# Optimization experiments

Measured on AMD Instinct MI355X. Metric: run time of the kernel, lower is better.

The kernel has to match this reference:

```python
import jax, jax.numpy as jnp
import numpy as np

E = 8          # num_experts
TOP_K = 2      # router top-k
ALPHA = 1.702  # swigluoai alpha
LIMIT = 7.0    # swigluoai clamp limit


def setup_inputs() -> dict:
    key = jax.random.key(0)
    ks = jax.random.split(key, 7)
    B, S, H, I = 2, 1024, 1024, 1024
    s = 1.0 / np.sqrt(H)  # keep activations O(1), realistic init scale
    return {
        "x": jax.random.normal(ks[0], (B, S, H), jnp.float32),
        "router_weight": jax.random.normal(ks[1], (E, H), jnp.float32) * s,
        "router_bias": jax.random.normal(ks[2], (E,), jnp.float32) * 0.01,
        "w1": jax.random.normal(ks[3], (E, H, 2 * I), jnp.float32) * s,  # interleaved gate/up
        "w1_bias": jax.random.normal(ks[4], (E, 2 * I), jnp.float32) * 0.01,
        "w2": jax.random.normal(ks[5], (E, I, H), jnp.float32) * s,
        "w2_bias": jax.random.normal(ks[6], (E, H), jnp.float32) * 0.01,
    }


def _moe(x, router_weight, router_bias, w1, w1_bias, w2, w2_bias):
    B, S, H = x.shape
    xf = x.reshape(-1, H)                                   # [T, H]
    # ---- router: softmax over expert logits, then top-k ----
    logits = xf @ router_weight.T + router_bias             # [T, E]
    probs = jax.nn.softmax(logits, axis=-1)
    expert_weights, expert_ids = jax.lax.top_k(probs, TOP_K)  # [T, k]
    # combine weights scattered to dense [T, E] (no normalization: normalize_expert_weights=None)
    combine = jnp.sum(jax.nn.one_hot(expert_ids, E, dtype=xf.dtype)
                      * expert_weights[..., None], axis=1)  # [T, E]
    # ---- grouped MLP, expressed densely per expert (reference semantics) ----
    h = jnp.einsum('th,ehi->eti', xf, w1) + w1_bias[:, None, :]   # [E, T, 2I]
    gate = h[..., 0::2]                                          # interleaved layout
    up = h[..., 1::2]
    gate = jnp.minimum(gate, LIMIT)                              # swigluoai: clamp gate max
    up = jnp.clip(up, -LIMIT, LIMIT)                             # clamp up both sides
    glu = gate * jax.nn.sigmoid(gate * ALPHA)
    act = (up + 1.0) * glu                                       # [E, T, I]
    y = jnp.einsum('eti,eih->eth', act, w2) + w2_bias[:, None, :]  # [E, T, H]
    out = jnp.einsum('eth,te->th', y, combine)                   # weighted combine
    return out.reshape(B, S, H), expert_weights


def reference(x, router_weight, router_bias, w1, w1_bias, w2, w2_bias):
    return _moe(x, router_weight, router_bias, w1, w1_bias, w2, w2_bias)
```

## Files before the change

### kernel.cpp

```cpp
#include <hip/hip_runtime.h>
#include <cstdint>
#include <cstddef>

typedef unsigned short u16;
typedef short bf16x8 __attribute__((ext_vector_type(8)));
typedef float floatx4 __attribute__((ext_vector_type(4)));

#define GLD16(gp, sp) __builtin_amdgcn_global_load_lds(                      \
    (const __attribute__((address_space(1))) void*)(gp),                     \
    (__attribute__((address_space(3))) void*)(sp), 16, 0, 0)

__device__ __forceinline__ u16 f2bf(float f) {
  unsigned u = __float_as_uint(f);
  u += 0x7fffu + ((u >> 16) & 1u);
  return (u16)(u >> 16);
}

__global__ void cvt_x_kernel(const float4* __restrict__ in, u16* __restrict__ out, int n4) {
  int i = blockIdx.x * blockDim.x + threadIdx.x;
  if (i >= n4) return;
  float4 v = in[i];
  ushort4 o;
  o.x = f2bf(v.x); o.y = f2bf(v.y); o.z = f2bf(v.z); o.w = f2bf(v.w);
  ((ushort4*)out)[i] = o;
}

__global__ void transpose_cvt_kernel(const float* __restrict__ in, u16* __restrict__ out,
                                     int R, int C) {
  __shared__ float tile[32][33];
  size_t base = (size_t)blockIdx.z * (size_t)R * (size_t)C;
  int c0 = blockIdx.x * 32, r0 = blockIdx.y * 32;
  int tx = threadIdx.x, ty = threadIdx.y;
#pragma unroll
  for (int k = 0; k < 32; k += 8)
    tile[ty + k][tx] = in[base + (size_t)(r0 + ty + k) * C + (c0 + tx)];
  __syncthreads();
#pragma unroll
  for (int k = 0; k < 32; k += 8)
    out[base + (size_t)(c0 + ty + k) * R + (r0 + tx)] = f2bf(tile[tx][ty + k]);
}

__global__ void router_kernel(const float* __restrict__ x, const float* __restrict__ rw,
                              const float* __restrict__ rb, float* __restrict__ ew,
                              int* __restrict__ eids, float* __restrict__ eprobs) {
  const int wave = threadIdx.x >> 6, lane = threadIdx.x & 63;
  const int t = blockIdx.x * 4 + wave;
  const float4* xv = (const float4*)(x + (size_t)t * 1024);
  float acc[8];
#pragma unroll
  for (int e = 0; e < 8; ++e) acc[e] = 0.f;
  for (int j = lane; j < 256; j += 64) {
    float4 xx = xv[j];
#pragma unroll
    for (int e = 0; e < 8; ++e) {
      float4 wv = ((const float4*)(rw + (size_t)e * 1024))[j];
      acc[e] += xx.x * wv.x + xx.y * wv.y + xx.z * wv.z + xx.w * wv.w;
    }
  }
#pragma unroll
  for (int e = 0; e < 8; ++e) {
    float v = acc[e];
#pragma unroll
    for (int off = 32; off > 0; off >>= 1) v += __shfl_down(v, off);
    acc[e] = v;
  }
  if (lane == 0) {
    float p[8];
    float mx = -1e30f;
#pragma unroll
    for (int e = 0; e < 8; ++e) { p[e] = acc[e] + rb[e]; mx = fmaxf(mx, p[e]); }
    float sum = 0.f;
#pragma unroll
    for (int e = 0; e < 8; ++e) { p[e] = __expf(p[e] - mx); sum += p[e]; }
    float inv = 1.f / sum;
#pragma unroll
    for (int e = 0; e < 8; ++e) p[e] *= inv;
    int i0 = 0;
#pragma unroll
    for (int e = 1; e < 8; ++e) if (p[e] > p[i0]) i0 = e;
    int i1 = (i0 == 0) ? 1 : 0;
#pragma unroll
    for (int e = 0; e < 8; ++e) if (e != i0 && e != i1 && p[e] > p[i1]) i1 = e;
    ew[t * 2 + 0] = p[i0];
    ew[t * 2 + 1] = p[i1];
    eids[t * 2 + 0] = i0;
    eids[t * 2 + 1] = i1;
    eprobs[t * 2 + 0] = p[i0];
    eprobs[t * 2 + 1] = p[i1];
  }
}

__global__ void build_lists_kernel(const int* __restrict__ eids, const float* __restrict__ eprobs,
                                   int* __restrict__ row_token, float* __restrict__ row_scale,
                                   int* __restrict__ meta) {
  __shared__ int cnt[8], base[8], cur[8];
  const int tid = threadIdx.x;
  if (tid < 8) { cnt[tid] = 0; cur[tid] = 0; }
  __syncthreads();
  for (int t = tid; t < 2048; t += 256) {
    atomicAdd(&cnt[eids[t * 2 + 0]], 1);
    atomicAdd(&cnt[eids[t * 2 + 1]], 1);
  }
  __syncthreads();
  if (tid == 0) {
    int off = 0, w = 0;
    for (int e = 0; e < 8; ++e) {
      base[e] = off;
      meta[48 + e] = off;
      int nb = (cnt[e] + 127) >> 7;
      for (int rb = 0; rb < nb; ++rb) meta[1 + w++] = (e << 8) | rb;
      off += nb << 7;
    }
    meta[0] = w;
  }
  __syncthreads();
  for (int s = tid; s < 5120; s += 256) { row_token[s] = -1; row_scale[s] = 0.f; }
  __syncthreads();
  for (int t = tid; t < 2048; t += 256) {
#pragma unroll
    for (int k = 0; k < 2; ++k) {
      int e = eids[t * 2 + k];
      int s = base[e] + atomicAdd(&cur[e], 1);
      row_token[s] = t;
      row_scale[s] = eprobs[t * 2 + k];
    }
  }
}

__global__ void bias_init_kernel(const int* __restrict__ eids, const float* __restrict__ eprobs,
                                 const float* __restrict__ w2b, float* __restrict__ out) {
  int idx = blockIdx.x * 256 + threadIdx.x;
  int t = idx >> 10, h = idx & 1023;
  int e0 = eids[t * 2], e1 = eids[t * 2 + 1];
  out[idx] = eprobs[t * 2] * w2b[e0 * 1024 + h] + eprobs[t * 2 + 1] * w2b[e1 * 1024 + h];
}

__global__ __launch_bounds__(256) void gemm1_act_kernel(
    const u16* __restrict__ xb, const u16* __restrict__ w1t,
    const float* __restrict__ w1b,
    const int* __restrict__ row_token, const float* __restrict__ row_scale,
    const int* __restrict__ meta, u16* __restrict__ actS) {
  if ((int)blockIdx.x >= meta[0]) return;
  __shared__ __align__(16) u16 As[128 * 32];
  __shared__ __align__(16) u16 Bs[128 * 32];
  const int w = meta[1 + blockIdx.x];
  const int e = w >> 8, rb = w & 255;
  const int slotB = meta[48 + e] + rb * 128;
  const int colBase = blockIdx.y * 128;
  const int tid = threadIdx.x, lane = tid & 63, wave = tid >> 6;
  const int row16 = lane & 15, chunk = lane >> 4;
  const u16* Bt = w1t + (size_t)e * 2048 * 1024;
  const u16* aP[2]; const u16* bP[2];
#pragma unroll
  for (int r = 0; r < 2; ++r) {
    int g = r * 4 + wave;
    int tk = row_token[slotB + g * 16 + row16];
    if (tk < 0) tk = 0;
    aP[r] = xb + (size_t)tk * 1024 + chunk * 8;
    bP[r] = Bt + (size_t)(colBase + g * 16 + row16) * 1024 + chunk * 8;
  }
  const int wr = wave >> 1, wc = wave & 1;
  floatx4 acc[4][4];
#pragma unroll
  for (int mi = 0; mi < 4; ++mi)
#pragma unroll
    for (int ni = 0; ni < 4; ++ni) acc[mi][ni] = floatx4{0.f, 0.f, 0.f, 0.f};

  for (int kt = 0; kt < 32; ++kt) {
    const int k = kt * 32;
    GLD16(aP[0] + k, As + wave * 512);
    GLD16(bP[0] + k, Bs + wave * 512);
    GLD16(aP[1] + k, As + (4 + wave) * 512);
    GLD16(bP[1] + k, Bs + (4 + wave) * 512);
    __syncthreads();
    bf16x8 af[4], bfr[4];
#pragma unroll
    for (int mi = 0; mi < 4; ++mi) af[mi] = *(const bf16x8*)(As + (wr * 4 + mi) * 512 + lane * 8);
#pragma unroll
    for (int ni = 0; ni < 4; ++ni) bfr[ni] = *(const bf16x8*)(Bs + (wc * 4 + ni) * 512 + lane * 8);
#pragma unroll
    for (int mi = 0; mi < 4; ++mi)
#pragma unroll
      for (int ni = 0; ni < 4; ++ni)
        acc[mi][ni] = __builtin_amdgcn_mfma_f32_16x16x32_bf16(af[mi], bfr[ni], acc[mi][ni], 0, 0, 0);
    __syncthreads();
  }

  const int cl = lane & 15, ql = lane >> 4;
#pragma unroll
  for (int mi = 0; mi < 4; ++mi) {
#pragma unroll
    for (int r = 0; r < 4; ++r) {
      const int slot = slotB + wr * 64 + mi * 16 + ql * 4 + r;
      const float c = row_scale[slot];
#pragma unroll
      for (int ni = 0; ni < 4; ++ni) {
        const int n = colBase + wc * 64 + ni * 16 + cl;
        float v = acc[mi][ni][r] + w1b[e * 2048 + n];
        float o = __shfl_xor(v, 1);
        if ((lane & 1) == 0) {
          float g = fminf(v, 7.f);
          float u = fminf(fmaxf(o, -7.f), 7.f);
          float sg = 1.f / (1.f + __expf(-1.702f * g));
          float a = (u + 1.f) * (g * sg);
          actS[(size_t)slot * 1024 + (n >> 1)] = f2bf(c * a);
        }
      }
    }
  }
}

__global__ __launch_bounds__(256) void gemm2_add_kernel(
    const u16* __restrict__ actS, const u16* __restrict__ w2t,
    const int* __restrict__ row_token, const int* __restrict__ meta,
    float* __restrict__ out) {
  if ((int)blockIdx.x >= meta[0]) return;
  __shared__ __align__(16) u16 As[128 * 32];
  __shared__ __align__(16) u16 Bs[128 * 32];
  const int w = meta[1 + blockIdx.x];
  const int e = w >> 8, rb = w & 255;
  const int slotB = meta[48 + e] + rb * 128;
  const int colBase = blockIdx.y * 128;
  const int tid = threadIdx.x, lane = tid & 63, wave = tid >> 6;
  const int row16 = lane & 15, chunk = lane >> 4;
  const u16* Bt = w2t + (size_t)e * 1024 * 1024;
  const u16* aP[2]; const u16* bP[2];
#pragma unroll
  for (int r = 0; r < 2; ++r) {
    int g = r * 4 + wave;
    aP[r] = actS + (size_t)(slotB + g * 16 + row16) * 1024 + chunk * 8;
    bP[r] = Bt + (size_t)(colBase + g * 16 + row16) * 1024 + chunk * 8;
  }
  const int wr = wave >> 1, wc = wave & 1;
  floatx4 acc[4][4];
#pragma unroll
  for (int mi = 0; mi < 4; ++mi)
#pragma unroll
    for (int ni = 0; ni < 4; ++ni) acc[mi][ni] = floatx4{0.f, 0.f, 0.f, 0.f};

  for (int kt = 0; kt < 32; ++kt) {
    const int k = kt * 32;
    GLD16(aP[0] + k, As + wave * 512);
    GLD16(bP[0] + k, Bs + wave * 512);
    GLD16(aP[1] + k, As + (4 + wave) * 512);
    GLD16(bP[1] + k, Bs + (4 + wave) * 512);
    __syncthreads();
    bf16x8 af[4], bfr[4];
#pragma unroll
    for (int mi = 0; mi < 4; ++mi) af[mi] = *(const bf16x8*)(As + (wr * 4 + mi) * 512 + lane * 8);
#pragma unroll
    for (int ni = 0; ni < 4; ++ni) bfr[ni] = *(const bf16x8*)(Bs + (wc * 4 + ni) * 512 + lane * 8);
#pragma unroll
    for (int mi = 0; mi < 4; ++mi)
#pragma unroll
      for (int ni = 0; ni < 4; ++ni)
        acc[mi][ni] = __builtin_amdgcn_mfma_f32_16x16x32_bf16(af[mi], bfr[ni], acc[mi][ni], 0, 0, 0);
    __syncthreads();
  }

  const int cl = lane & 15, ql = lane >> 4;
#pragma unroll
  for (int mi = 0; mi < 4; ++mi)
#pragma unroll
    for (int r = 0; r < 4; ++r) {
      const int slot = slotB + wr * 64 + mi * 16 + ql * 4 + r;
      const int tok = row_token[slot];
      if (tok < 0) continue;
#pragma unroll
      for (int ni = 0; ni < 4; ++ni) {
        const int col = colBase + wc * 64 + ni * 16 + cl;
        atomicAdd(out + (size_t)tok * 1024 + col, acc[mi][ni][r]);
      }
    }
}

extern "C" void kernel_launch(void* const* d_in, const int* in_sizes, int n_in,
                              void* d_out, int out_size, void* d_ws, size_t ws_size,
                              hipStream_t stream) {
  const float* x   = (const float*)d_in[0];
  const float* rw  = (const float*)d_in[1];
  const float* rb  = (const float*)d_in[2];
  const float* w1  = (const float*)d_in[3];
  const float* w1b = (const float*)d_in[4];
  const float* w2  = (const float*)d_in[5];
  const float* w2b = (const float*)d_in[6];
  float* out = (float*)d_out;
  float* ew  = out + (size_t)2048 * 1024;

  char* ws = (char*)d_ws;
  u16* xb        = (u16*)(ws);
  u16* w1t       = (u16*)(ws + (4ull << 20));
  u16* w2t       = (u16*)(ws + (36ull << 20));
  u16* actS      = (u16*)(ws + (52ull << 20));
  int* eids      = (int*)(ws + (62ull << 20));
  float* eprobs  = (float*)(ws + (62ull << 20) + (16 << 10));
  int* row_token = (int*)(ws + (62ull << 20) + (32 << 10));
  float* row_scale = (float*)(ws + (62ull << 20) + (52 << 10));
  int* meta      = (int*)(ws + (62ull << 20) + (72 << 10));

  cvt_x_kernel<<<2048, 256, 0, stream>>>((const float4*)x, xb, 2048 * 1024 / 4);
  transpose_cvt_kernel<<<dim3(64, 32, 8), dim3(32, 8), 0, stream>>>(w1, w1t, 1024, 2048);
  transpose_cvt_kernel<<<dim3(32, 32, 8), dim3(32, 8), 0, stream>>>(w2, w2t, 1024, 1024);
  router_kernel<<<512, 256, 0, stream>>>(x, rw, rb, ew, eids, eprobs);
  build_lists_kernel<<<1, 256, 0, stream>>>(eids, eprobs, row_token, row_scale, meta);
  bias_init_kernel<<<8192, 256, 0, stream>>>(eids, eprobs, w2b, out);
  gemm1_act_kernel<<<dim3(40, 16), 256, 0, stream>>>(xb, w1t, w1b, row_token, row_scale, meta, actS);
  gemm2_add_kernel<<<dim3(40, 8), 256, 0, stream>>>(actS, w2t, row_token, meta, out);
}
```

Baseline: 272.6 us.

## Double-buffer LDS in both expert GEMMs and replace atomic scatter with combine kernel

Both grouped GEMM kernels now use two LDS buffers, so the global-to-LDS load for the next K tile is issued while the MFMAs run on the current one, and one barrier per step is removed. GEMM2 writes per-slot outputs to a float scratch buffer (aliased over the w1t region, which is dead by then) instead of doing float atomicAdd into the output. A new combine kernel gathers the two expert rows per token via a token-to-slot map and adds the weighted biases, replacing the bias-init kernel. This trades atomic contention for an extra round trip of roughly 20 MB of scratch traffic.

Measured after the change: 282.2 us. 1.04x slower.

```diff
diff --git a/kernel.cpp b/kernel.cpp
--- a/kernel.cpp
+++ b/kernel.cpp
@@ -92,7 +92,7 @@
 
 __global__ void build_lists_kernel(const int* __restrict__ eids, const float* __restrict__ eprobs,
                                    int* __restrict__ row_token, float* __restrict__ row_scale,
-                                   int* __restrict__ meta) {
+                                   int* __restrict__ tok2slot, int* __restrict__ meta) {
   __shared__ int cnt[8], base[8], cur[8];
   const int tid = threadIdx.x;
   if (tid < 8) { cnt[tid] = 0; cur[tid] = 0; }
@@ -123,16 +123,9 @@
       int s = base[e] + atomicAdd(&cur[e], 1);
       row_token[s] = t;
       row_scale[s] = eprobs[t * 2 + k];
-    }
-  }
-}
-
-__global__ void bias_init_kernel(const int* __restrict__ eids, const float* __restrict__ eprobs,
-                                 const float* __restrict__ w2b, float* __restrict__ out) {
-  int idx = blockIdx.x * 256 + threadIdx.x;
-  int t = idx >> 10, h = idx & 1023;
-  int e0 = eids[t * 2], e1 = eids[t * 2 + 1];
-  out[idx] = eprobs[t * 2] * w2b[e0 * 1024 + h] + eprobs[t * 2 + 1] * w2b[e1 * 1024 + h];
+      tok2slot[t * 2 + k] = s;
+    }
+  }
 }
 
 __global__ __launch_bounds__(256) void gemm1_act_kernel(
@@ -141,8 +134,10 @@
     const int* __restrict__ row_token, const float* __restrict__ row_scale,
     const int* __restrict__ meta, u16* __restrict__ actS) {
   if ((int)blockIdx.x >= meta[0]) return;
-  __shared__ __align__(16) u16 As[128 * 32];
-  __shared__ __align__(16) u16 Bs[128 * 32];
+  __shared__ __align__(16) u16 As0[128 * 32];
+  __shared__ __align__(16) u16 Bs0[128 * 32];
+  __shared__ __align__(16) u16 As1[128 * 32];
+  __shared__ __align__(16) u16 Bs1[128 * 32];
   const int w = meta[1 + blockIdx.x];
   const int e = w >> 8, rb = w & 255;
   const int slotB = meta[48 + e] + rb * 128;
@@ -166,24 +161,52 @@
 #pragma unroll
     for (int ni = 0; ni < 4; ++ni) acc[mi][ni] = floatx4{0.f, 0.f, 0.f, 0.f};
 
-  for (int kt = 0; kt < 32; ++kt) {
-    const int k = kt * 32;
-    GLD16(aP[0] + k, As + wave * 512);
-    GLD16(bP[0] + k, Bs + wave * 512);
-    GLD16(aP[1] + k, As + (4 + wave) * 512);
-    GLD16(bP[1] + k, Bs + (4 + wave) * 512);
-    __syncthreads();
-    bf16x8 af[4], bfr[4];
-#pragma unroll
-    for (int mi = 0; mi < 4; ++mi) af[mi] = *(const bf16x8*)(As + (wr * 4 + mi) * 512 + lane * 8);
-#pragma unroll
-    for (int ni = 0; ni < 4; ++ni) bfr[ni] = *(const bf16x8*)(Bs + (wc * 4 + ni) * 512 + lane * 8);
-#pragma unroll
-    for (int mi = 0; mi < 4; ++mi)
-#pragma unroll
-      for (int ni = 0; ni < 4; ++ni)
-        acc[mi][ni] = __builtin_amdgcn_mfma_f32_16x16x32_bf16(af[mi], bfr[ni], acc[mi][ni], 0, 0, 0);
-    __syncthreads();
+  GLD16(aP[0], As0 + wave * 512);
+  GLD16(bP[0], Bs0 + wave * 512);
+  GLD16(aP[1], As0 + (4 + wave) * 512);
+  GLD16(bP[1], Bs0 + (4 + wave) * 512);
+  __syncthreads();
+
+#pragma unroll 1
+  for (int kt = 0; kt < 32; kt += 2) {
+    {
+      bf16x8 af[4], bfr[4];
+#pragma unroll
+      for (int mi = 0; mi < 4; ++mi) af[mi] = *(const bf16x8*)(As0 + (wr * 4 + mi) * 512 + lane * 8);
+#pragma unroll
+      for (int ni = 0; ni < 4; ++ni) bfr[ni] = *(const bf16x8*)(Bs0 + (wc * 4 + ni) * 512 + lane * 8);
+      const int k = (kt + 1) * 32;
+      GLD16(aP[0] + k, As1 + wave * 512);
+      GLD16(bP[0] + k, Bs1 + wave * 512);
+      GLD16(aP[1] + k, As1 + (4 + wave) * 512);
+      GLD16(bP[1] + k, Bs1 + (4 + wave) * 512);
+#pragma unroll
+      for (int mi = 0; mi < 4; ++mi)
+#pragma unroll
+        for (int ni = 0; ni < 4; ++ni)
+          acc[mi][ni] = __builtin_amdgcn_mfma_f32_16x16x32_bf16(af[mi], bfr[ni], acc[mi][ni], 0, 0, 0);
+      __syncthreads();
+    }
+    {
+      bf16x8 af[4], bfr[4];
+#pragma unroll
+      for (int mi = 0; mi < 4; ++mi) af[mi] = *(const bf16x8*)(As1 + (wr * 4 + mi) * 512 + lane * 8);
+#pragma unroll
+      for (int ni = 0; ni < 4; ++ni) bfr[ni] = *(const bf16x8*)(Bs1 + (wc * 4 + ni) * 512 + lane * 8);
+      if (kt + 2 < 32) {
+        const int k = (kt + 2) * 32;
+        GLD16(aP[0] + k, As0 + wave * 512);
+        GLD16(bP[0] + k, Bs0 + wave * 512);
+        GLD16(aP[1] + k, As0 + (4 + wave) * 512);
+        GLD16(bP[1] + k, Bs0 + (4 + wave) * 512);
+      }
+#pragma unroll
+      for (int mi = 0; mi < 4; ++mi)
+#pragma unroll
+        for (int ni = 0; ni < 4; ++ni)
+          acc[mi][ni] = __builtin_amdgcn_mfma_f32_16x16x32_bf16(af[mi], bfr[ni], acc[mi][ni], 0, 0, 0);
+      __syncthreads();
+    }
   }
 
   const int cl = lane & 15, ql = lane >> 4;
@@ -210,13 +233,14 @@
   }
 }
 
-__global__ __launch_bounds__(256) void gemm2_add_kernel(
+__global__ __launch_bounds__(256) void gemm2_kernel(
     const u16* __restrict__ actS, const u16* __restrict__ w2t,
-    const int* __restrict__ row_token, const int* __restrict__ meta,
-    float* __restrict__ out) {
+    const int* __restrict__ meta, float* __restrict__ y) {
   if ((int)blockIdx.x >= meta[0]) return;
-  __shared__ __align__(16) u16 As[128 * 32];
-  __shared__ __align__(16) u16 Bs[128 * 32];
+  __shared__ __align__(16) u16 As0[128 * 32];
+  __shared__ __align__(16) u16 Bs0[128 * 32];
+  __shared__ __align__(16) u16 As1[128 * 32];
+  __shared__ __align__(16) u16 Bs1[128 * 32];
   const int w = meta[1 + blockIdx.x];
   const int e = w >> 8, rb = w & 255;
   const int slotB = meta[48 + e] + rb * 128;
@@ -238,24 +262,52 @@
 #pragma unroll
     for (int ni = 0; ni < 4; ++ni) acc[mi][ni] = floatx4{0.f, 0.f, 0.f, 0.f};
 
-  for (int kt = 0; kt < 32; ++kt) {
-    const int k = kt * 32;
-    GLD16(aP[0] + k, As + wave * 512);
-    GLD16(bP[0] + k, Bs + wave * 512);
-    GLD16(aP[1] + k, As + (4 + wave) * 512);
-    GLD16(bP[1] + k, Bs + (4 + wave) * 512);
-    __syncthreads();
-    bf16x8 af[4], bfr[4];
-#pragma unroll
-    for (int mi = 0; mi < 4; ++mi) af[mi] = *(const bf16x8*)(As + (wr * 4 + mi) * 512 + lane * 8);
-#pragma unroll
-    for (int ni = 0; ni < 4; ++ni) bfr[ni] = *(const bf16x8*)(Bs + (wc * 4 + ni) * 512 + lane * 8);
-#pragma unroll
-    for (int mi = 0; mi < 4; ++mi)
-#pragma unroll
-      for (int ni = 0; ni < 4; ++ni)
-        acc[mi][ni] = __builtin_amdgcn_mfma_f32_16x16x32_bf16(af[mi], bfr[ni], acc[mi][ni], 0, 0, 0);
-    __syncthreads();
+  GLD16(aP[0], As0 + wave * 512);
+  GLD16(bP[0], Bs0 + wave * 512);
+  GLD16(aP[1], As0 + (4 + wave) * 512);
+  GLD16(bP[1], Bs0 + (4 + wave) * 512);
+  __syncthreads();
+
+#pragma unroll 1
+  for (int kt = 0; kt < 32; kt += 2) {
+    {
+      bf16x8 af[4], bfr[4];
+#pragma unroll
+      for (int mi = 0; mi < 4; ++mi) af[mi] = *(const bf16x8*)(As0 + (wr * 4 + mi) * 512 + lane * 8);
+#pragma unroll
+      for (int ni = 0; ni < 4; ++ni) bfr[ni] = *(const bf16x8*)(Bs0 + (wc * 4 + ni) * 512 + lane * 8);
+      const int k = (kt + 1) * 32;
+      GLD16(aP[0] + k, As1 + wave * 512);
+      GLD16(bP[0] + k, Bs1 + wave * 512);
+      GLD16(aP[1] + k, As1 + (4 + wave) * 512);
+      GLD16(bP[1] + k, Bs1 + (4 + wave) * 512);
+#pragma unroll
+      for (int mi = 0; mi < 4; ++mi)
+#pragma unroll
+        for (int ni = 0; ni < 4; ++ni)
+          acc[mi][ni] = __builtin_amdgcn_mfma_f32_16x16x32_bf16(af[mi], bfr[ni], acc[mi][ni], 0, 0, 0);
+      __syncthreads();
+    }
+    {
+      bf16x8 af[4], bfr[4];
+#pragma unroll
+      for (int mi = 0; mi < 4; ++mi) af[mi] = *(const bf16x8*)(As1 + (wr * 4 + mi) * 512 + lane * 8);
+#pragma unroll
+      for (int ni = 0; ni < 4; ++ni) bfr[ni] = *(const bf16x8*)(Bs1 + (wc * 4 + ni) * 512 + lane * 8);
+      if (kt + 2 < 32) {
+        const int k = (kt + 2) * 32;
+        GLD16(aP[0] + k, As0 + wave * 512);
+        GLD16(bP[0] + k, Bs0 + wave * 512);
+        GLD16(aP[1] + k, As0 + (4 + wave) * 512);
+        GLD16(bP[1] + k, Bs0 + (4 + wave) * 512);
+      }
+#pragma unroll
+      for (int mi = 0; mi < 4; ++mi)
+#pragma unroll
+        for (int ni = 0; ni < 4; ++ni)
+          acc[mi][ni] = __builtin_amdgcn_mfma_f32_16x16x32_bf16(af[mi], bfr[ni], acc[mi][ni], 0, 0, 0);
+      __syncthreads();
+    }
   }
 
   const int cl = lane & 15, ql = lane >> 4;
@@ -264,14 +316,23 @@
 #pragma unroll
     for (int r = 0; r < 4; ++r) {
       const int slot = slotB + wr * 64 + mi * 16 + ql * 4 + r;
-      const int tok = row_token[slot];
-      if (tok < 0) continue;
 #pragma unroll
       for (int ni = 0; ni < 4; ++ni) {
         const int col = colBase + wc * 64 + ni * 16 + cl;
-        atomicAdd(out + (size_t)tok * 1024 + col, acc[mi][ni][r]);
+        y[(size_t)slot * 1024 + col] = acc[mi][ni][r];
       }
     }
+}
+
+__global__ void combine_kernel(const float* __restrict__ y, const int* __restrict__ eids,
+                               const float* __restrict__ eprobs, const int* __restrict__ tok2slot,
+                               const float* __restrict__ w2b, float* __restrict__ out) {
+  int idx = blockIdx.x * 256 + threadIdx.x;
+  int t = idx >> 10, h = idx & 1023;
+  int e0 = eids[t * 2], e1 = eids[t * 2 + 1];
+  int s0 = tok2slot[t * 2], s1 = tok2slot[t * 2 + 1];
+  out[idx] = eprobs[t * 2] * w2b[e0 * 1024 + h] + eprobs[t * 2 + 1] * w2b[e1 * 1024 + h]
+           + y[(size_t)s0 * 1024 + h] + y[(size_t)s1 * 1024 + h];
 }
 
 extern "C" void kernel_launch(void* const* d_in, const int* in_sizes, int n_in,
@@ -290,6 +351,7 @@
   char* ws = (char*)d_ws;
   u16* xb        = (u16*)(ws);
   u16* w1t       = (u16*)(ws + (4ull << 20));
+  float* y       = (float*)(ws + (4ull << 20));
   u16* w2t       = (u16*)(ws + (36ull << 20));
   u16* actS      = (u16*)(ws + (52ull << 20));
   int* eids      = (int*)(ws + (62ull << 20));
@@ -297,13 +359,14 @@
   int* row_token = (int*)(ws + (62ull << 20) + (32 << 10));
   float* row_scale = (float*)(ws + (62ull << 20) + (52 << 10));
   int* meta      = (int*)(ws + (62ull << 20) + (72 << 10));
+  int* tok2slot  = (int*)(ws + (62ull << 20) + (74 << 10));
 
   cvt_x_kernel<<<2048, 256, 0, stream>>>((const float4*)x, xb, 2048 * 1024 / 4);
   transpose_cvt_kernel<<<dim3(64, 32, 8), dim3(32, 8), 0, stream>>>(w1, w1t, 1024, 2048);
   transpose_cvt_kernel<<<dim3(32, 32, 8), dim3(32, 8), 0, stream>>>(w2, w2t, 1024, 1024);
   router_kernel<<<512, 256, 0, stream>>>(x, rw, rb, ew, eids, eprobs);
-  build_lists_kernel<<<1, 256, 0, stream>>>(eids, eprobs, row_token, row_scale, meta);
-  bias_init_kernel<<<8192, 256, 0, stream>>>(eids, eprobs, w2b, out);
+  build_lists_kernel<<<1, 256, 0, stream>>>(eids, eprobs, row_token, row_scale, tok2slot, meta);
   gemm1_act_kernel<<<dim3(40, 16), 256, 0, stream>>>(xb, w1t, w1b, row_token, row_scale, meta, actS);
-  gemm2_add_kernel<<<dim3(40, 8), 256, 0, stream>>>(actS, w2t, row_token, meta, out);
-}
+  gemm2_kernel<<<dim3(40, 8), 256, 0, stream>>>(actS, w2t, meta, y);
+  combine_kernel<<<8192, 256, 0, stream>>>(y, eids, eprobs, tok2slot, w2b, out);
+}
```
